# Performance work log

Hardware: AMD Instinct MI355X
Metric: run time of the kernel (lower is better)

Reference implementation:

```python
import jax, jax.numpy as jnp
import numpy as np

N_EVENTS = 200_000
M_TYPES = 64
K_KERNELS = 4
T_VAL = 100.0


def setup_inputs() -> dict:
    key = jax.random.key(0)
    k1, k2, k3, k4, k5 = jax.random.split(key, 5)
    # sorted event times in (0, T)
    t = jnp.sort(jax.random.uniform(k1, (N_EVENTS,), dtype=jnp.float32)) * T_VAL
    ti = t.reshape(1, N_EVENTS, 1)
    mi = jax.random.randint(k2, (N_EVENTS,), 0, M_TYPES)
    # positive Hawkes parameters (stability: row sums of alpha < 1)
    mu = 0.1 + 0.5 * jax.random.uniform(k3, (M_TYPES,), dtype=jnp.float32)
    alpha = (0.5 / M_TYPES) * jax.random.uniform(k4, (K_KERNELS, M_TYPES, M_TYPES), dtype=jnp.float32)
    gamma = 0.5 + jax.random.uniform(k5, (K_KERNELS,), dtype=jnp.float32)
    return {"mu": mu, "alpha": alpha, "gamma": gamma, "ti": ti, "mi": mi, "T": 100}


def _decay_states(gamma, t, mi, M):
    """Prefix-scan states h[i, m', k] = exp(-gamma_k*dt_i) * (h[i-1, m', k] + 1{m_{i-1}=m'}).
    Matches alpha_transition_matrices / prefix_scan(state_mult) in HawkesNLL.backward."""
    dt = jnp.concatenate([jnp.zeros((1,), t.dtype), t[1:] - t[:-1]])          # (N,)
    decay = jnp.exp(-gamma[None, :] * dt[:, None])                            # (N, K)
    oh = jnp.concatenate([jnp.zeros((1, M), t.dtype),
                          jax.nn.one_hot(mi[:-1], M, dtype=t.dtype)], axis=0)  # (N, M)
    a = jnp.broadcast_to(decay[:, None, :], (t.shape[0], M, decay.shape[1]))  # (N, M, K)
    b = decay[:, None, :] * oh[:, :, None]                                    # (N, M, K)

    def combine(x, y):
        a1, b1 = x
        a2, b2 = y
        return a1 * a2, a2 * b1 + b2

    _, h = jax.lax.associative_scan(combine, (a, b), axis=0)
    return h                                                                  # (N, M, K)


def _nll(mu, alpha, gamma, ti, mi, T):
    t = ti.reshape(-1)                        # (N,)
    N = t.shape[0]
    M = alpha.shape[1]
    h = _decay_states(gamma, t, mi, M)        # (N, M, K)
    # intensity at each event: lam_i = mu[m_i] + sum_{k,m'} gamma_k * alpha[k, m', m_i] * h[i, m', k]
    lam = mu[mi] + jnp.einsum('kmn,nmk,k->n', alpha[:, :, mi], h, gamma)      # (N,)
    # compensator: T*sum(mu) + sum_{j,k,p} alpha[k, m_j, p] * (1 - exp(-gamma_k (T - t_j)))
    asum = alpha.sum(axis=2)                                                  # (K, M)
    surv = -jnp.expm1(-gamma[None, :] * (T - t)[:, None])                     # (N, K)
    comp = T * mu.sum() + jnp.sum(asum[:, mi].T * surv)
    return (-jnp.sum(jnp.log(lam)) + comp) / N


def reference(mu, alpha, gamma, ti, mi, T):
    return _nll(mu, alpha, gamma, ti, mi, jnp.float32(T))
```

## Files before the change

### kernel.cpp

```cpp
#include <hip/hip_runtime.h>

#define MT 64
#define KK 4
#define NBK 4096
#define MAXB 49

__device__ __forceinline__ float wredf(float v) {
  #pragma unroll
  for (int off = 32; off > 0; off >>= 1) v += __shfl_xor(v, off, 64);
  return v;
}
__device__ __forceinline__ double wredd(double v) {
  #pragma unroll
  for (int off = 32; off > 0; off >>= 1) v += __shfl_xor(v, off, 64);
  return v;
}
__device__ __forceinline__ float4 f4fma(float4 a, float4 b, float4 c) {
  return make_float4(fmaf(a.x,b.x,c.x), fmaf(a.y,b.y,c.y),
                     fmaf(a.z,b.z,c.z), fmaf(a.w,b.w,c.w));
}
__device__ __forceinline__ float4 f4mul(float4 a, float4 b) {
  return make_float4(a.x*b.x, a.y*b.y, a.z*b.z, a.w*b.w);
}
__device__ __forceinline__ float parse_T(const int* Tp) {
  int v = *Tp;
  if (v >= 1 && v <= 1000000000) return (float)v;
  return __int_as_float(v);
}

__global__ __launch_bounds__(512, 4) void k_phase1(
    const float* __restrict__ t, const int* __restrict__ mi,
    const float* __restrict__ alpha, const float* __restrict__ gamma,
    const int* __restrict__ Tp,
    float4* __restrict__ cd4G, float* __restrict__ slG,
    float4* __restrict__ Cl8, float4* __restrict__ Dc8,
    float4* __restrict__ Ag, float4* __restrict__ gdec,
    float* __restrict__ compP, int N, int B)
{
  __shared__ float4 AT4[MT*MT];
  __shared__ __align__(16) unsigned char pool[8320];
  __shared__ float sL[8*MAXB];
  __shared__ float4 asumS[MT];
  __shared__ float red[8];
  float4*        d4t = (float4*)pool;
  unsigned char* miL = pool + 8*MAXB*16;
  float4*        cw  = (float4*)pool;
  float4*        cwd = (float4*)(pool + 8192);

  const int tid = threadIdx.x, lane = tid & 63, wv = tid >> 6;
  const float g0=gamma[0], g1=gamma[1], g2=gamma[2], g3=gamma[3];

  #pragma unroll
  for (int idx = tid; idx < MT*MT; idx += 512) {
    float a0=alpha[idx],         a1=alpha[MT*MT+idx];
    float a2=alpha[2*MT*MT+idx], a3=alpha[3*MT*MT+idx];
    AT4[idx] = make_float4(g0*a0, g1*a1, g2*a2, g3*a3);
  }
  if (tid < MT*KK) {
    const int m = tid >> 2, k = tid & 3;
    const float4* row = (const float4*)(alpha + (size_t)k*MT*MT + m*MT);
    float s = 0.f;
    #pragma unroll
    for (int j = 0; j < MT/4; ++j) { float4 v = row[j]; s += (v.x+v.y)+(v.z+v.w); }
    ((float*)asumS)[(m<<2)+k] = s;
  }
  __syncthreads();

  const float T = parse_T(Tp);
  const int s0w = (int)blockIdx.x * 8 * B;
  const int b  = (int)blockIdx.x*8 + wv;
  const int s0 = b*B, e0 = min(N, s0+B);
  float4 q = make_float4(0.f,0.f,0.f,0.f);
  float comp = 0.f;
  const int nch = (B + MAXB - 1) / MAXB;

  for (int ch = 0; ch < nch; ++ch) {
    const int c0 = ch*MAXB;
    const int cb = min(B - c0, MAXB);
    const int tot = 8*cb;
    for (int jj = tid; jj < tot; jj += 512) {
      int w = jj / cb, lo = jj - w*cb;
      int i = s0w + w*B + c0 + lo;
      if (i < N) {
        float ti = t[i];
        float tp = (i > 0) ? t[i-1] : ti;
        float dt = ti - tp;
        d4t[jj] = make_float4(__expf(-g0*dt), __expf(-g1*dt),
                              __expf(-g2*dt), __expf(-g3*dt));
        int m = mi[i];
        miL[jj] = (unsigned char)m;
        int refi = s0w + w*B - 1;
        float tr = (refi >= 0) ? t[refi] : t[0];
        float x = ti - tr;
        cd4G[i] = make_float4(__expf(-g0*x), __expf(-g1*x),
                              __expf(-g2*x), __expf(-g3*x));
        float y = T - ti;
        float4 as = asumS[m];
        comp = fmaf(as.x, 1.f-__expf(-g0*y), comp);
        comp = fmaf(as.y, 1.f-__expf(-g1*y), comp);
        comp = fmaf(as.z, 1.f-__expf(-g2*y), comp);
        comp = fmaf(as.w, 1.f-__expf(-g3*y), comp);
      }
    }
    __syncthreads();
    const int iend = min(cb, e0 - s0 - c0);
    int j = wv*cb;
    #pragma unroll 4
    for (int ii = 0; ii < iend; ++ii, ++j) {
      float4 d = d4t[j];
      int m = miL[j];
      float4 a = AT4[(m<<6) + lane];
      float s = q.x*d.x; s=fmaf(q.y,d.y,s); s=fmaf(q.z,d.z,s); s=fmaf(q.w,d.w,s);
      if (lane == m) sL[j] = s;
      q = f4fma(q, d, a);
    }
    __syncthreads();
    for (int jj = tid; jj < tot; jj += 512) {
      int w = jj / cb, lo = jj - w*cb;
      int i = s0w + w*B + c0 + lo;
      if (i < N) slG[i] = sL[jj];
    }
    __syncthreads();
  }

  comp = wredf(comp);
  if (lane == 0) red[wv] = comp;

  float4 df = make_float4(1.f,1.f,1.f,1.f);
  if (lane == 0) {
    int last  = max(e0-1, 0);
    int plast = min(max(s0-1, 0), N-1);
    float dtb = t[last] - t[plast];
    df = make_float4(__expf(-g0*dtb),__expf(-g1*dtb),
                     __expf(-g2*dtb),__expf(-g3*dtb));
  }
  cw[wv*64 + lane] = q;
  if (lane == 0) cwd[wv] = df;
  __syncthreads();

  float4 c  = make_float4(0.f,0.f,0.f,0.f);
  float4 dp = make_float4(1.f,1.f,1.f,1.f);
  float4 Cl = c, Dc = dp;
  #pragma unroll
  for (int jo = 0; jo < 8; ++jo) {
    if (jo == wv) { Cl = c; Dc = dp; }
    float4 d = cwd[jo];
    float4 P = cw[jo*64 + lane];
    c  = f4fma(c, d, P);
    dp = f4mul(dp, d);
  }
  Cl8[(size_t)b*64 + lane] = Cl;
  if (lane == 0) Dc8[b] = Dc;
  if (wv == 0) {
    Ag[(size_t)blockIdx.x*64 + lane] = c;
    if (lane == 0) gdec[blockIdx.x] = dp;
    if (lane == 0) {
      float cc = 0.f;
      #pragma unroll
      for (int jr = 0; jr < 8; ++jr) cc += red[jr];
      compP[blockIdx.x] = cc;
    }
  }
}

__global__ __launch_bounds__(64) void k_scan2(
    const float4* __restrict__ Ag, const float4* __restrict__ gdec,
    float4* __restrict__ SgG, float4* __restrict__ sdecG)
{
  const int lane = threadIdx.x;
  const int s = blockIdx.x;
  float4 c  = make_float4(0.f,0.f,0.f,0.f);
  float4 dp = make_float4(1.f,1.f,1.f,1.f);
  const int o0 = s*32;
  #pragma unroll
  for (int bb = 0; bb < 4; ++bb) {
    float4 av[8], gv[8];
    #pragma unroll
    for (int j = 0; j < 8; ++j) {
      const int o = o0 + bb*8 + j;
      av[j] = Ag[(size_t)o*64 + lane];
      gv[j] = gdec[o];
    }
    #pragma unroll
    for (int j = 0; j < 8; ++j) {
      c  = f4fma(c, gv[j], av[j]);
      dp = f4mul(dp, gv[j]);
    }
  }
  SgG[(size_t)s*64 + lane] = c;
  if (lane == 0) sdecG[s] = dp;
}

__global__ __launch_bounds__(512, 4) void k_lam(
    const int* __restrict__ mi, const float* __restrict__ mu,
    const float4* __restrict__ cd4G, const float* __restrict__ slG,
    const float4* __restrict__ Cl8, const float4* __restrict__ Dc8,
    const float4* __restrict__ Ag, const float4* __restrict__ gdec,
    const float4* __restrict__ SgG, const float4* __restrict__ sdecG,
    float* __restrict__ npt, int N, int B)
{
  __shared__ float4 TopL[64];
  __shared__ float4 gpL[64];
  __shared__ float4 gdLs;
  __shared__ float red[8];
  const int tid = threadIdx.x, lane = tid & 63, wv = tid >> 6;
  const int oct = blockIdx.x;
  const int sup = oct >> 5;
  const int BPW = 8*B;
  const int i = oct*BPW + tid;

  int   m = 0;
  float4 cd, Cl, Dc; float sl = 0.f, muv = 0.f;
  const bool valid = (tid < BPW) && (i < N);
  if (valid) {
    m  = mi[i];
    cd = cd4G[i];
    sl = slG[i];
    muv = mu[m];
    int bl = tid / B;
    int b = oct*8 + bl;
    Dc = Dc8[b];
    Cl = Cl8[(size_t)b*64 + m];
  }

  if (wv == 0) {
    float4 tc = make_float4(0.f,0.f,0.f,0.f);
    int s = 0;
    for (; s + 4 <= sup; s += 4) {
      float4 av[4], gv[4];
      #pragma unroll
      for (int j = 0; j < 4; ++j) {
        av[j] = SgG[(size_t)(s+j)*64 + lane];
        gv[j] = sdecG[s+j];
      }
      #pragma unroll
      for (int j = 0; j < 4; ++j) tc = f4fma(tc, gv[j], av[j]);
    }
    for (; s < sup; ++s) tc = f4fma(tc, sdecG[s], SgG[(size_t)s*64 + lane]);
    TopL[lane] = tc;
  } else if (wv == 1) {
    float4 gp = make_float4(0.f,0.f,0.f,0.f);
    float4 gd = make_float4(1.f,1.f,1.f,1.f);
    int o = sup << 5;
    for (; o + 4 <= oct; o += 4) {
      float4 av[4], gv[4];
      #pragma unroll
      for (int j = 0; j < 4; ++j) {
        av[j] = Ag[(size_t)(o+j)*64 + lane];
        gv[j] = gdec[o+j];
      }
      #pragma unroll
      for (int j = 0; j < 4; ++j) {
        gp = f4fma(gp, gv[j], av[j]);
        gd = f4mul(gd, gv[j]);
      }
    }
    for (; o < oct; ++o) {
      gp = f4fma(gp, gdec[o], Ag[(size_t)o*64 + lane]);
      gd = f4mul(gd, gdec[o]);
    }
    gpL[lane] = gp;
    if (lane == 0) gdLs = gd;
  }
  __syncthreads();

  float v = 0.f;
  if (valid) {
    float4 coct = f4fma(gdLs, TopL[m], gpL[m]);
    float4 C = f4fma(Dc, coct, Cl);
    float lam = muv + sl + (C.x*cd.x + C.y*cd.y + C.z*cd.z + C.w*cd.w);
    v = __log2f(lam);
  }
  v = wredf(v);
  if (lane == 0) red[wv] = v;
  __syncthreads();
  if (tid == 0) {
    float s = 0.f;
    #pragma unroll
    for (int j = 0; j < 8; ++j) s += red[j];
    npt[oct] = s;
  }
}

__global__ __launch_bounds__(512) void k_final(
    const float* __restrict__ mu, const int* __restrict__ Tp,
    const float* __restrict__ compP, int nc,
    const float* __restrict__ npt, int nn,
    float* __restrict__ out, int N)
{
  const int tid = threadIdx.x;
  double sc = 0.0, sn = 0.0;
  for (int i = tid; i < nc; i += 512) sc += (double)compP[i];
  for (int i = tid; i < nn; i += 512) sn += (double)npt[i];
  double sm = (tid < MT) ? (double)mu[tid] : 0.0;
  sc = wredd(sc); sn = wredd(sn); sm = wredd(sm);
  __shared__ double s3[3][8];
  const int wv = tid >> 6, lane = tid & 63;
  if (lane == 0) { s3[0][wv]=sc; s3[1][wv]=sn; s3[2][wv]=sm; }
  __syncthreads();
  if (tid == 0) {
    double C=0.0, L=0.0, Mm=0.0;
    #pragma unroll
    for (int j = 0; j < 8; ++j) { C+=s3[0][j]; L+=s3[1][j]; Mm+=s3[2][j]; }
    L *= 0.6931471805599453;
    double T = (double)parse_T(Tp);
    out[0] = (float)((C + T*Mm - L) / (double)N);
  }
}

extern "C" void kernel_launch(void* const* d_in, const int* in_sizes, int n_in,
                              void* d_out, int out_size, void* d_ws, size_t ws_size,
                              hipStream_t stream)
{
  const float* mu    = (const float*)d_in[0];
  const float* alpha = (const float*)d_in[1];
  const float* gamma = (const float*)d_in[2];
  const float* t     = (const float*)d_in[3];
  const int*   mi    = (const int*)d_in[4];
  const int*   Tp    = (const int*)d_in[5];
  const int N = in_sizes[3];
  const int B   = (N + NBK - 1) / NBK;
  const int NOG = NBK / 8;

  float* p = (float*)d_ws;
  float4* cd4G  = (float4*)p; p += (size_t)N*4;
  float*  slG   = p;          p += ((size_t)N + 3) & ~(size_t)3;
  float4* Cl8   = (float4*)p; p += (size_t)NBK*256;
  float4* Dc8   = (float4*)p; p += (size_t)NBK*4;
  float4* Ag    = (float4*)p; p += (size_t)NOG*256;
  float4* gdec  = (float4*)p; p += (size_t)NOG*4;
  float4* SgG   = (float4*)p; p += (size_t)16*256;
  float4* sdecG = (float4*)p; p += (size_t)16*4;
  float*  compP = p;          p += NOG;
  float*  npt   = p;          p += NOG;

  k_phase1<<<NOG, 512, 0, stream>>>(t, mi, alpha, gamma, Tp, cd4G, slG,
                                    Cl8, Dc8, Ag, gdec, compP, N, B);
  k_scan2 <<<16,  64,  0, stream>>>(Ag, gdec, SgG, sdecG);
  k_lam   <<<NOG, 512, 0, stream>>>(mi, mu, cd4G, slG, Cl8, Dc8, Ag, gdec,
                                    SgG, sdecG, npt, N, B);
  k_final <<<1,   512, 0, stream>>>(mu, Tp, compP, NOG, npt, NOG,
                                    (float*)d_out, N);
}
```

Measured before the change: 32.70 us.

## Fold second-level scan into lambda kernel, recomputing super-block carries per block

```diff
diff --git a/kernel.cpp b/kernel.cpp
--- a/kernel.cpp
+++ b/kernel.cpp
@@ -163,46 +163,20 @@
   }
 }
 
-__global__ __launch_bounds__(64) void k_scan2(
-    const float4* __restrict__ Ag, const float4* __restrict__ gdec,
-    float4* __restrict__ SgG, float4* __restrict__ sdecG)
-{
-  const int lane = threadIdx.x;
-  const int s = blockIdx.x;
-  float4 c  = make_float4(0.f,0.f,0.f,0.f);
-  float4 dp = make_float4(1.f,1.f,1.f,1.f);
-  const int o0 = s*32;
-  #pragma unroll
-  for (int bb = 0; bb < 4; ++bb) {
-    float4 av[8], gv[8];
-    #pragma unroll
-    for (int j = 0; j < 8; ++j) {
-      const int o = o0 + bb*8 + j;
-      av[j] = Ag[(size_t)o*64 + lane];
-      gv[j] = gdec[o];
-    }
-    #pragma unroll
-    for (int j = 0; j < 8; ++j) {
-      c  = f4fma(c, gv[j], av[j]);
-      dp = f4mul(dp, gv[j]);
-    }
-  }
-  SgG[(size_t)s*64 + lane] = c;
-  if (lane == 0) sdecG[s] = dp;
-}
-
-__global__ __launch_bounds__(512, 4) void k_lam(
+__global__ __launch_bounds__(512, 4) void k_lam3(
     const int* __restrict__ mi, const float* __restrict__ mu,
     const float4* __restrict__ cd4G, const float* __restrict__ slG,
     const float4* __restrict__ Cl8, const float4* __restrict__ Dc8,
     const float4* __restrict__ Ag, const float4* __restrict__ gdec,
-    const float4* __restrict__ SgG, const float4* __restrict__ sdecG,
     float* __restrict__ npt, int N, int B)
 {
+  __shared__ float4 SgL[16*64];
+  __shared__ float4 sdecL[16];
   __shared__ float4 TopL[64];
   __shared__ float4 gpL[64];
   __shared__ float4 gdLs;
   __shared__ float red[8];
+
   const int tid = threadIdx.x, lane = tid & 63, wv = tid >> 6;
   const int oct = blockIdx.x;
   const int sup = oct >> 5;
@@ -223,20 +197,34 @@
     Cl = Cl8[(size_t)b*64 + m];
   }
 
+  for (int s = wv; s < sup; s += 8) {
+    float4 c  = make_float4(0.f,0.f,0.f,0.f);
+    float4 dp = make_float4(1.f,1.f,1.f,1.f);
+    const int o0 = s*32;
+    #pragma unroll
+    for (int bb = 0; bb < 4; ++bb) {
+      float4 av[8], gv[8];
+      #pragma unroll
+      for (int j = 0; j < 8; ++j) {
+        const int o = o0 + bb*8 + j;
+        av[j] = Ag[(size_t)o*64 + lane];
+        gv[j] = gdec[o];
+      }
+      #pragma unroll
+      for (int j = 0; j < 8; ++j) {
+        c  = f4fma(c, gv[j], av[j]);
+        dp = f4mul(dp, gv[j]);
+      }
+    }
+    SgL[s*64 + lane] = c;
+    if (lane == 0) sdecL[s] = dp;
+  }
+  __syncthreads();
+
   if (wv == 0) {
     float4 tc = make_float4(0.f,0.f,0.f,0.f);
-    int s = 0;
-    for (; s + 4 <= sup; s += 4) {
-      float4 av[4], gv[4];
-      #pragma unroll
-      for (int j = 0; j < 4; ++j) {
-        av[j] = SgG[(size_t)(s+j)*64 + lane];
-        gv[j] = sdecG[s+j];
-      }
-      #pragma unroll
-      for (int j = 0; j < 4; ++j) tc = f4fma(tc, gv[j], av[j]);
-    }
-    for (; s < sup; ++s) tc = f4fma(tc, sdecG[s], SgG[(size_t)s*64 + lane]);
+    for (int s = 0; s < sup; ++s)
+      tc = f4fma(tc, sdecL[s], SgL[s*64 + lane]);
     TopL[lane] = tc;
   } else if (wv == 1) {
     float4 gp = make_float4(0.f,0.f,0.f,0.f);
@@ -329,16 +317,13 @@
   float4* Dc8   = (float4*)p; p += (size_t)NBK*4;
   float4* Ag    = (float4*)p; p += (size_t)NOG*256;
   float4* gdec  = (float4*)p; p += (size_t)NOG*4;
-  float4* SgG   = (float4*)p; p += (size_t)16*256;
-  float4* sdecG = (float4*)p; p += (size_t)16*4;
   float*  compP = p;          p += NOG;
   float*  npt   = p;          p += NOG;
 
   k_phase1<<<NOG, 512, 0, stream>>>(t, mi, alpha, gamma, Tp, cd4G, slG,
                                     Cl8, Dc8, Ag, gdec, compP, N, B);
-  k_scan2 <<<16,  64,  0, stream>>>(Ag, gdec, SgG, sdecG);
-  k_lam   <<<NOG, 512, 0, stream>>>(mi, mu, cd4G, slG, Cl8, Dc8, Ag, gdec,
-                                    SgG, sdecG, npt, N, B);
+  k_lam3  <<<NOG, 512, 0, stream>>>(mi, mu, cd4G, slG, Cl8, Dc8, Ag, gdec,
+                                    npt, N, B);
   k_final <<<1,   512, 0, stream>>>(mu, Tp, compP, NOG, npt, NOG,
                                     (float*)d_out, N);
 }
```

Result: slower. 51.09 us (+56.3%).

## Replace sequential intra-block scan with rescaled sums and per-event direct reductions

Applied to the files above, without the earlier changes.

```diff
diff --git a/kernel.cpp b/kernel.cpp
--- a/kernel.cpp
+++ b/kernel.cpp
@@ -3,7 +3,7 @@
 #define MT 64
 #define KK 4
 #define NBK 4096
-#define MAXB 49
+#define MAXB 52
 
 __device__ __forceinline__ float wredf(float v) {
   #pragma unroll
@@ -32,20 +32,19 @@
     const float* __restrict__ t, const int* __restrict__ mi,
     const float* __restrict__ alpha, const float* __restrict__ gamma,
     const int* __restrict__ Tp,
-    float4* __restrict__ cd4G, float* __restrict__ slG,
+    float* __restrict__ slG,
     float4* __restrict__ Cl8, float4* __restrict__ Dc8,
     float4* __restrict__ Ag, float4* __restrict__ gdec,
     float* __restrict__ compP, int N, int B)
 {
   __shared__ float4 AT4[MT*MT];
   __shared__ __align__(16) unsigned char pool[8320];
-  __shared__ float sL[8*MAXB];
   __shared__ float4 asumS[MT];
   __shared__ float red[8];
-  float4*        d4t = (float4*)pool;
-  unsigned char* miL = pool + 8*MAXB*16;
-  float4*        cw  = (float4*)pool;
-  float4*        cwd = (float4*)(pool + 8192);
+  float4*        rcpt = (float4*)pool;
+  unsigned char* miL  = pool + 8*MAXB*16;
+  float4*        cw   = (float4*)pool;
+  float4*        cwd  = (float4*)(pool + 8192);
 
   const int tid = threadIdx.x, lane = tid & 63, wv = tid >> 6;
   const float g0=gamma[0], g1=gamma[1], g2=gamma[2], g3=gamma[3];
@@ -68,63 +67,74 @@
 
   const float T = parse_T(Tp);
   const int s0w = (int)blockIdx.x * 8 * B;
+  const int tot = 8 * B;
+
+  int   mI = 0, lo = 0, bl = 0;
+  float xI = 0.f;
+  float comp = 0.f;
+  const int iG = s0w + tid;
+  const bool evOK = (tid < tot) && (iG < N);
+  if (evOK) {
+    bl = tid / B; lo = tid - bl*B;
+    float ti = t[iG];
+    int refi = s0w + bl*B - 1;
+    float tr = (refi >= 0) ? t[refi] : t[0];
+    xI = ti - tr;
+    rcpt[tid] = make_float4(__expf(g0*xI), __expf(g1*xI),
+                            __expf(g2*xI), __expf(g3*xI));
+    mI = mi[iG];
+    miL[tid] = (unsigned char)mI;
+    float y = T - ti;
+    float4 as = asumS[mI];
+    comp = fmaf(as.x, 1.f-__expf(-g0*y), comp);
+    comp = fmaf(as.y, 1.f-__expf(-g1*y), comp);
+    comp = fmaf(as.z, 1.f-__expf(-g2*y), comp);
+    comp = fmaf(as.w, 1.f-__expf(-g3*y), comp);
+  }
+  comp = wredf(comp);
+  if (lane == 0) red[wv] = comp;
+  __syncthreads();
+
   const int b  = (int)blockIdx.x*8 + wv;
   const int s0 = b*B, e0 = min(N, s0+B);
-  float4 q = make_float4(0.f,0.f,0.f,0.f);
-  float comp = 0.f;
-  const int nch = (B + MAXB - 1) / MAXB;
-
-  for (int ch = 0; ch < nch; ++ch) {
-    const int c0 = ch*MAXB;
-    const int cb = min(B - c0, MAXB);
-    const int tot = 8*cb;
-    for (int jj = tid; jj < tot; jj += 512) {
-      int w = jj / cb, lo = jj - w*cb;
-      int i = s0w + w*B + c0 + lo;
-      if (i < N) {
-        float ti = t[i];
-        float tp = (i > 0) ? t[i-1] : ti;
-        float dt = ti - tp;
-        d4t[jj] = make_float4(__expf(-g0*dt), __expf(-g1*dt),
-                              __expf(-g2*dt), __expf(-g3*dt));
-        int m = mi[i];
-        miL[jj] = (unsigned char)m;
-        int refi = s0w + w*B - 1;
-        float tr = (refi >= 0) ? t[refi] : t[0];
-        float x = ti - tr;
-        cd4G[i] = make_float4(__expf(-g0*x), __expf(-g1*x),
-                              __expf(-g2*x), __expf(-g3*x));
-        float y = T - ti;
-        float4 as = asumS[m];
-        comp = fmaf(as.x, 1.f-__expf(-g0*y), comp);
-        comp = fmaf(as.y, 1.f-__expf(-g1*y), comp);
-        comp = fmaf(as.z, 1.f-__expf(-g2*y), comp);
-        comp = fmaf(as.w, 1.f-__expf(-g3*y), comp);
-      }
-    }
-    __syncthreads();
-    const int iend = min(cb, e0 - s0 - c0);
-    int j = wv*cb;
+  const int iend = max(e0 - s0, 0);
+  float4 S = make_float4(0.f,0.f,0.f,0.f);
+  {
+    const int base = wv*B;
     #pragma unroll 4
-    for (int ii = 0; ii < iend; ++ii, ++j) {
-      float4 d = d4t[j];
-      int m = miL[j];
+    for (int ii = 0; ii < iend; ++ii) {
+      float4 r = rcpt[base + ii];
+      int m = miL[base + ii];
       float4 a = AT4[(m<<6) + lane];
-      float s = q.x*d.x; s=fmaf(q.y,d.y,s); s=fmaf(q.z,d.z,s); s=fmaf(q.w,d.w,s);
-      if (lane == m) sL[j] = s;
-      q = f4fma(q, d, a);
-    }
-    __syncthreads();
-    for (int jj = tid; jj < tot; jj += 512) {
-      int w = jj / cb, lo = jj - w*cb;
-      int i = s0w + w*B + c0 + lo;
-      if (i < N) slG[i] = sL[jj];
-    }
-    __syncthreads();
-  }
-
-  comp = wredf(comp);
-  if (lane == 0) red[wv] = comp;
+      S = f4fma(a, r, S);
+    }
+  }
+  float4 q;
+  {
+    float xl = 0.f;
+    if (iend > 0) {
+      int refi = s0 - 1;
+      float tr = (refi >= 0) ? t[refi] : t[0];
+      xl = t[e0-1] - tr;
+    }
+    float4 cdl = make_float4(__expf(-g0*xl), __expf(-g1*xl),
+                             __expf(-g2*xl), __expf(-g3*xl));
+    q = f4mul(S, cdl);
+  }
+
+  if (evOK) {
+    const int jb = bl*B;
+    float4 S4 = make_float4(0.f,0.f,0.f,0.f);
+    for (int jj = 0; jj < lo; ++jj) {
+      int mj = miL[jb + jj];
+      float4 r = rcpt[jb + jj];
+      float4 a = AT4[(mj<<6) + mI];
+      S4 = f4fma(a, r, S4);
+    }
+    float4 cdi = make_float4(__expf(-g0*xI), __expf(-g1*xI),
+                             __expf(-g2*xI), __expf(-g3*xI));
+    slG[iG] = S4.x*cdi.x + S4.y*cdi.y + S4.z*cdi.z + S4.w*cdi.w;
+  }
 
   float4 df = make_float4(1.f,1.f,1.f,1.f);
   if (lane == 0) {
@@ -134,6 +144,7 @@
     df = make_float4(__expf(-g0*dtb),__expf(-g1*dtb),
                      __expf(-g2*dtb),__expf(-g3*dtb));
   }
+  __syncthreads();
   cw[wv*64 + lane] = q;
   if (lane == 0) cwd[wv] = df;
   __syncthreads();
@@ -192,8 +203,9 @@
 }
 
 __global__ __launch_bounds__(512, 4) void k_lam(
-    const int* __restrict__ mi, const float* __restrict__ mu,
-    const float4* __restrict__ cd4G, const float* __restrict__ slG,
+    const float* __restrict__ t, const int* __restrict__ mi,
+    const float* __restrict__ gamma, const float* __restrict__ mu,
+    const float* __restrict__ slG,
     const float4* __restrict__ Cl8, const float4* __restrict__ Dc8,
     const float4* __restrict__ Ag, const float4* __restrict__ gdec,
     const float4* __restrict__ SgG, const float4* __restrict__ sdecG,
@@ -214,11 +226,16 @@
   const bool valid = (tid < BPW) && (i < N);
   if (valid) {
     m  = mi[i];
-    cd = cd4G[i];
     sl = slG[i];
     muv = mu[m];
     int bl = tid / B;
     int b = oct*8 + bl;
+    float ti = t[i];
+    int refi = b*B - 1;
+    float tr = (refi >= 0) ? t[refi] : t[0];
+    float x = ti - tr;
+    const float g0=gamma[0], g1=gamma[1], g2=gamma[2], g3=gamma[3];
+    cd = make_float4(__expf(-g0*x), __expf(-g1*x), __expf(-g2*x), __expf(-g3*x));
     Dc = Dc8[b];
     Cl = Cl8[(size_t)b*64 + m];
   }
@@ -323,7 +340,6 @@
   const int NOG = NBK / 8;
 
   float* p = (float*)d_ws;
-  float4* cd4G  = (float4*)p; p += (size_t)N*4;
   float*  slG   = p;          p += ((size_t)N + 3) & ~(size_t)3;
   float4* Cl8   = (float4*)p; p += (size_t)NBK*256;
   float4* Dc8   = (float4*)p; p += (size_t)NBK*4;
@@ -334,10 +350,10 @@
   float*  compP = p;          p += NOG;
   float*  npt   = p;          p += NOG;
 
-  k_phase1<<<NOG, 512, 0, stream>>>(t, mi, alpha, gamma, Tp, cd4G, slG,
+  k_phase1<<<NOG, 512, 0, stream>>>(t, mi, alpha, gamma, Tp, slG,
                                     Cl8, Dc8, Ag, gdec, compP, N, B);
   k_scan2 <<<16,  64,  0, stream>>>(Ag, gdec, SgG, sdecG);
-  k_lam   <<<NOG, 512, 0, stream>>>(mi, mu, cd4G, slG, Cl8, Dc8, Ag, gdec,
+  k_lam   <<<NOG, 512, 0, stream>>>(t, mi, gamma, mu, slG, Cl8, Dc8, Ag, gdec,
                                     SgG, sdecG, npt, N, B);
   k_final <<<1,   512, 0, stream>>>(mu, Tp, compP, NOG, npt, NOG,
                                     (float*)d_out, N);
```

Measured after the change: 35.51 us. +8.6%, slower.

## Recompute per-event decay factors in k_lam instead of storing cd4G

Applied to the files above, without the earlier changes.

```diff
diff --git a/kernel.cpp b/kernel.cpp
--- a/kernel.cpp
+++ b/kernel.cpp
@@ -32,7 +32,7 @@
     const float* __restrict__ t, const int* __restrict__ mi,
     const float* __restrict__ alpha, const float* __restrict__ gamma,
     const int* __restrict__ Tp,
-    float4* __restrict__ cd4G, float* __restrict__ slG,
+    float* __restrict__ slG,
     float4* __restrict__ Cl8, float4* __restrict__ Dc8,
     float4* __restrict__ Ag, float4* __restrict__ gdec,
     float* __restrict__ compP, int N, int B)
@@ -89,11 +89,6 @@
                               __expf(-g2*dt), __expf(-g3*dt));
         int m = mi[i];
         miL[jj] = (unsigned char)m;
-        int refi = s0w + w*B - 1;
-        float tr = (refi >= 0) ? t[refi] : t[0];
-        float x = ti - tr;
-        cd4G[i] = make_float4(__expf(-g0*x), __expf(-g1*x),
-                              __expf(-g2*x), __expf(-g3*x));
         float y = T - ti;
         float4 as = asumS[m];
         comp = fmaf(as.x, 1.f-__expf(-g0*y), comp);
@@ -192,8 +187,9 @@
 }
 
 __global__ __launch_bounds__(512, 4) void k_lam(
-    const int* __restrict__ mi, const float* __restrict__ mu,
-    const float4* __restrict__ cd4G, const float* __restrict__ slG,
+    const float* __restrict__ t, const int* __restrict__ mi,
+    const float* __restrict__ gamma, const float* __restrict__ mu,
+    const float* __restrict__ slG,
     const float4* __restrict__ Cl8, const float4* __restrict__ Dc8,
     const float4* __restrict__ Ag, const float4* __restrict__ gdec,
     const float4* __restrict__ SgG, const float4* __restrict__ sdecG,
@@ -202,25 +198,28 @@
   __shared__ float4 TopL[64];
   __shared__ float4 gpL[64];
   __shared__ float4 gdLs;
+  __shared__ float4 C_L[8*64];
   __shared__ float red[8];
   const int tid = threadIdx.x, lane = tid & 63, wv = tid >> 6;
   const int oct = blockIdx.x;
   const int sup = oct >> 5;
   const int BPW = 8*B;
   const int i = oct*BPW + tid;
+  const float g0=gamma[0], g1=gamma[1], g2=gamma[2], g3=gamma[3];
 
   int   m = 0;
-  float4 cd, Cl, Dc; float sl = 0.f, muv = 0.f;
+  float4 cd; float sl = 0.f, muv = 0.f;
   const bool valid = (tid < BPW) && (i < N);
   if (valid) {
     m  = mi[i];
-    cd = cd4G[i];
     sl = slG[i];
     muv = mu[m];
     int bl = tid / B;
-    int b = oct*8 + bl;
-    Dc = Dc8[b];
-    Cl = Cl8[(size_t)b*64 + m];
+    float ti = t[i];
+    int refi = (oct*8 + bl)*B - 1;
+    float tr = (refi >= 0) ? t[refi] : t[0];
+    float x = ti - tr;
+    cd = make_float4(__expf(-g0*x), __expf(-g1*x), __expf(-g2*x), __expf(-g3*x));
   }
 
   if (wv == 0) {
@@ -264,10 +263,19 @@
   }
   __syncthreads();
 
+  {
+    const int bl2 = wv;
+    const int m2  = lane;
+    const int b2  = oct*8 + bl2;
+    float4 coct = f4fma(gdLs, TopL[m2], gpL[m2]);
+    C_L[(bl2<<6) + m2] = f4fma(Dc8[b2], coct, Cl8[(size_t)b2*64 + m2]);
+  }
+  __syncthreads();
+
   float v = 0.f;
   if (valid) {
-    float4 coct = f4fma(gdLs, TopL[m], gpL[m]);
-    float4 C = f4fma(Dc, coct, Cl);
+    int bl = tid / B;
+    float4 C = C_L[(bl<<6) + m];
     float lam = muv + sl + (C.x*cd.x + C.y*cd.y + C.z*cd.z + C.w*cd.w);
     v = __log2f(lam);
   }
@@ -323,7 +331,6 @@
   const int NOG = NBK / 8;
 
   float* p = (float*)d_ws;
-  float4* cd4G  = (float4*)p; p += (size_t)N*4;
   float*  slG   = p;          p += ((size_t)N + 3) & ~(size_t)3;
   float4* Cl8   = (float4*)p; p += (size_t)NBK*256;
   float4* Dc8   = (float4*)p; p += (size_t)NBK*4;
@@ -334,10 +341,10 @@
   float*  compP = p;          p += NOG;
   float*  npt   = p;          p += NOG;
 
-  k_phase1<<<NOG, 512, 0, stream>>>(t, mi, alpha, gamma, Tp, cd4G, slG,
+  k_phase1<<<NOG, 512, 0, stream>>>(t, mi, alpha, gamma, Tp, slG,
                                     Cl8, Dc8, Ag, gdec, compP, N, B);
   k_scan2 <<<16,  64,  0, stream>>>(Ag, gdec, SgG, sdecG);
-  k_lam   <<<NOG, 512, 0, stream>>>(mi, mu, cd4G, slG, Cl8, Dc8, Ag, gdec,
+  k_lam   <<<NOG, 512, 0, stream>>>(t, mi, gamma, mu, slG, Cl8, Dc8, Ag, gdec,
                                     SgG, sdecG, npt, N, B);
   k_final <<<1,   512, 0, stream>>>(mu, Tp, compP, NOG, npt, NOG,
                                     (float*)d_out, N);
```

Result: no change. 32.58 us (median of 2 runs) (-0.4%).
